# Kernel optimization log

Measured on AMD Instinct MI355X. Metric: run time of the kernel, lower is better.

Reference implementation:

```python
import jax, jax.numpy as jnp
import numpy as np

EP = 1e-4
MAX_ITER = 100
L = [512, 512]          # context lengths
C = 256                 # padded feature dim == total_dim
HEADS = 2


def nonsat_activation(x, ep=EP, max_iter=MAX_ITER):
    # Fixed-point iteration y <- (2y^3/3 + x)/(y^2+1), y0 = x.
    # Matches torch version: iterate on detached values, final update uses live x.
    xd = jax.lax.stop_gradient(x)
    f = lambda y: (2.0 * y ** 3 / 3.0 + xd) / (y ** 2 + 1.0)

    def cond(s):
        y, y_new, i = s
        return jnp.logical_and(jnp.mean(jnp.abs(y_new - y)) > ep, i <= max_iter)

    def body(s):
        y, y_new, i = s
        return (y_new, f(y_new), i + 1)

    y_prev, _, _ = jax.lax.while_loop(cond, body, (xd, f(xd), 0))
    y_prev = jax.lax.stop_gradient(y_prev)
    # final (returned) update, differentiable w.r.t. x only
    return (2.0 * y_prev ** 3 / 3.0 + x) / (y_prev ** 2 + 1.0)


def setup_inputs() -> dict:
    key = jax.random.key(0)
    k1, k2, k3 = jax.random.split(key, 3)
    x1 = jax.random.normal(k1, (32, 512, 256), dtype=jnp.float32)
    x2 = jax.random.normal(k2, (32, 512, 192), dtype=jnp.float32)
    # xavier_normal_ for U: std = sqrt(2/(fan_in+fan_out)) = sqrt(2/512) = 1/16
    U = jax.random.normal(k3, (HEADS, C, C), dtype=jnp.float32) * (1.0 / 16.0)
    return {"x1": x1, "x2": x2, "U": U}


def reference(x1, x2, U):
    # pad contexts to common feature dim C (zeros on the right)
    contexts = [x1, jnp.pad(x2, ((0, 0), (0, 0), (0, C - x2.shape[-1])))]
    q = sum(L)
    scaling = C ** (-0.5)
    M = jnp.concatenate(contexts, axis=1)  # (B, q, C)

    # mask uses sizes = L[1:] with blocks starting at offset 0 (faithful quirk)
    mask_mul = jnp.ones((q, q), dtype=jnp.float32).at[:L[1], :L[1]].set(0.0)

    h_reps = []
    mask_add = None
    for h in range(HEADS):
        # K[b,i,j] = sum_{c,d} M[b,i,c] U[h,c,d] M[b,j,d]
        K = jnp.einsum('bic,cd,bjd->bij', M, U[h], M) * scaling
        K = nonsat_activation(K)
        if mask_add is None:  # cached after head 0, reused for later heads
            mask_add = jnp.zeros((q, q), dtype=jnp.float32).at[:L[1], :L[1]].set(jnp.min(K))
        K_hat = K * mask_mul + mask_add
        cols = jnp.max(K_hat, axis=1)   # (B, q) max over rows per column
        rows = jnp.max(K_hat, axis=2)   # (B, q) max over cols per row
        alpha = rows + cols             # (B, q)
        reps = []
        offset = 0
        for i, Ci in enumerate(contexts):
            a = alpha[:, offset:offset + L[i]]          # (B, l_i)
            offset += L[i]
            wt = jax.nn.softmax(a, axis=1)              # (B, l_i)
            r = jnp.einsum('bl,blc->bc', wt, Ci)        # (B, C)
            reps.append(r)
        h_reps.append(jnp.stack(reps, axis=1))          # (B, N, C)
    return jnp.stack(h_reps, axis=0)                    # (heads, B, N, C)
```

## Files before the change

### kernel.cpp

```cpp
#include <hip/hip_runtime.h>
#include <math.h>

typedef _Float16 h16;
typedef h16  h16x8 __attribute__((ext_vector_type(8)));
typedef h16  h16x4 __attribute__((ext_vector_type(4)));
typedef float f32x4 __attribute__((ext_vector_type(4)));

#define MH_OFF   ((size_t)0)
#define ML_OFF   (MH_OFF + 16777216)
#define UHT_OFF  (ML_OFF + 16777216)
#define ULT_OFF  (UHT_OFF + 262144)
#define RMA_OFF  (ULT_OFF + 262144)
#define RMH_OFF  (RMA_OFF + 262144)
#define PCM_OFF  (RMH_OFF + 262144)
#define M0_OFF   (PCM_OFF + 4194304)

__device__ __forceinline__ float nonsat(float x) {
    float y = x;
#pragma unroll
    for (int i = 0; i < 24; ++i) {
        float y2 = y * y;
        y = fmaf(0.66666667f * y, y2, x) / (y2 + 1.0f);
    }
    return y;
}

__device__ __forceinline__ int fkey(float f) {
    const int i = __float_as_int(f);
    return (i >= 0) ? i : (i ^ 0x7fffffff);
}
__device__ __forceinline__ float funkey(int k) {
    return __int_as_float((k >= 0) ? k : (k ^ 0x7fffffff));
}

__global__ void k_prep(const float* __restrict__ x1, const float* __restrict__ x2,
                       const float* __restrict__ U, h16* __restrict__ MH,
                       h16* __restrict__ ML, h16* __restrict__ UHt,
                       h16* __restrict__ ULt, int* __restrict__ m0key,
                       float* __restrict__ out) {
    const int gid = blockIdx.x * 256 + threadIdx.x;
    if (blockIdx.x < 8192) {
        const int g  = gid;
        const int d4 = (g & 63) * 4;
        const int j  = (g >> 6) & 1023;
        const int b  = g >> 16;
        float v[4];
        if (j < 512) {
            const float4 p = *(const float4*)(x1 + ((size_t)(b * 512 + j) * 256 + d4));
            v[0] = p.x; v[1] = p.y; v[2] = p.z; v[3] = p.w;
        } else if (d4 < 192) {
            const float4 p = *(const float4*)(x2 +
                (size_t)(b * 512 + (j - 512)) * 192 + d4);
            v[0] = p.x; v[1] = p.y; v[2] = p.z; v[3] = p.w;
        } else {
            v[0] = v[1] = v[2] = v[3] = 0.0f;
        }
        h16x4 hh, ll;
#pragma unroll
        for (int k = 0; k < 4; ++k) {
            const h16 hi = (h16)v[k];
            hh[k] = hi;
            ll[k] = (h16)(v[k] - (float)hi);
        }
        const size_t o = (size_t)g * 4;
        *(h16x4*)&MH[o] = hh;
        *(h16x4*)&ML[o] = ll;
    } else if (blockIdx.x < 8320) {
        const int g  = gid - 8192 * 256;
        const int c4 = (g & 63) * 4;
        const int d  = (g >> 6) & 255;
        const int h  = g >> 14;
        h16x4 hh, ll;
#pragma unroll
        for (int k = 0; k < 4; ++k) {
            const float v = U[((size_t)h * 256 + c4 + k) * 256 + d] * 4.0f;
            const h16 hi = (h16)v;
            hh[k] = hi;
            ll[k] = (h16)(v - (float)hi);
        }
        const size_t o = ((size_t)h * 256 + d) * 256 + c4;
        *(h16x4*)&UHt[o] = hh;
        *(h16x4*)&ULt[o] = ll;
    } else {
        const int z = gid - 8320 * 256;
        out[z] = 0.0f;
        if (z == 0) *m0key = 0x7fffffff;
    }
}

__device__ __forceinline__ void stage_b(const h16* __restrict__ MH,
                                        const h16* __restrict__ ML,
                                        h16* sBf, int buf, int b, int jt,
                                        int jtile, int kc, int t, int w) {
    const int jrow0 = jt * 512 + jtile * 256;
    const int c = (t & 3) ^ ((t >> 3) & 3);
#pragma unroll
    for (int g = 0; g < 2; ++g) {
        const size_t src = (size_t)(b * 1024 + jrow0 + g * 128 + (t >> 2)) * 256
                           + kc * 32 + c * 8;
        h16* dH = sBf + (size_t)(buf * 2 + 0) * 8192 + g * 4096 + w * 512;
        h16* dL = sBf + (size_t)(buf * 2 + 1) * 8192 + g * 4096 + w * 512;
        __builtin_amdgcn_global_load_lds(
            (const __attribute__((address_space(1))) void*)(MH + src),
            (__attribute__((address_space(3))) void*)dH, 16, 0, 0);
        __builtin_amdgcn_global_load_lds(
            (const __attribute__((address_space(1))) void*)(ML + src),
            (__attribute__((address_space(3))) void*)dL, 16, 0, 0);
    }
}

__global__ __launch_bounds__(512, 2)
void k_main(const h16* __restrict__ MH, const h16* __restrict__ ML,
            const h16* __restrict__ UHt, const h16* __restrict__ ULt,
            float* __restrict__ rmax_all, float* __restrict__ rmax_hi,
            float* __restrict__ pcm, int* __restrict__ m0key) {
    __shared__ __align__(16) h16 sP[2][64 * 256];
    __shared__ __align__(16) h16 sB[2 * 2 * 8192];
    __shared__ float red[1024 + 8];
    __shared__ float scm[2][512];

    const int n    = blockIdx.x;
    const int x    = n & 7;
    const int s    = n >> 3;
    const int b    = x + 8 * (s >> 5);
    const int h    = (s >> 4) & 1;
    const int rblk = s & 15;
    const int hb   = h * 32 + b;
    const int r0   = rblk * 64;
    const int t    = threadIdx.x;
    const int w    = t >> 6;
    const int l    = t & 63;
    const int q    = l >> 4;
    const int ln   = l & 15;
    const int wr   = w >> 2;
    const int wj   = w & 3;

    const int jts    = (h == 1 && rblk < 8) ? 1 : 0;
    const int Usteps = (2 - jts) * 16;

    stage_b(MH, ML, sB, 0, b, jts, 0, 0, t, w);

    {
        const int wrA = w >> 2, wcA = w & 3;
        f32x4 accA[2][4];
        const f32x4 z4 = {0.f, 0.f, 0.f, 0.f};
#pragma unroll
        for (int i = 0; i < 2; ++i)
#pragma unroll
            for (int j2 = 0; j2 < 4; ++j2) accA[i][j2] = z4;

        for (int kc = 0; kc < 8; ++kc) {
            const int c0 = kc * 32;
            h16x8 aH[2], aL[2], bH[4], bL[4];
#pragma unroll
            for (int ti = 0; ti < 2; ++ti) {
                const size_t off =
                    (size_t)(b * 1024 + r0 + wrA * 32 + ti * 16 + ln) * 256 + c0 + q * 8;
                aH[ti] = *(const h16x8*)&MH[off];
                aL[ti] = *(const h16x8*)&ML[off];
            }
#pragma unroll
            for (int tj = 0; tj < 4; ++tj) {
                const size_t off =
                    (size_t)(h * 256 + wcA * 64 + tj * 16 + ln) * 256 + c0 + q * 8;
                bH[tj] = *(const h16x8*)&UHt[off];
                bL[tj] = *(const h16x8*)&ULt[off];
            }
#pragma unroll
            for (int ti = 0; ti < 2; ++ti)
#pragma unroll
                for (int tj = 0; tj < 4; ++tj)
                    accA[ti][tj] = __builtin_amdgcn_mfma_f32_16x16x32_f16(
                        aH[ti], bH[tj], accA[ti][tj], 0, 0, 0);
#pragma unroll
            for (int ti = 0; ti < 2; ++ti)
#pragma unroll
                for (int tj = 0; tj < 4; ++tj)
                    accA[ti][tj] = __builtin_amdgcn_mfma_f32_16x16x32_f16(
                        aL[ti], bH[tj], accA[ti][tj], 0, 0, 0);
#pragma unroll
            for (int ti = 0; ti < 2; ++ti)
#pragma unroll
                for (int tj = 0; tj < 4; ++tj)
                    accA[ti][tj] = __builtin_amdgcn_mfma_f32_16x16x32_f16(
                        aH[ti], bL[tj], accA[ti][tj], 0, 0, 0);
        }
#pragma unroll
        for (int ti = 0; ti < 2; ++ti)
#pragma unroll
            for (int tj = 0; tj < 4; ++tj)
#pragma unroll
                for (int reg = 0; reg < 4; ++reg) {
                    const int r = wrA * 32 + ti * 16 + q * 4 + reg;
                    const int d = wcA * 64 + tj * 16 + ln;
                    const float v = accA[ti][tj][reg];
                    const h16 hi = (h16)v;
                    const h16 lo = (h16)(v - (float)hi);
                    const int off = r * 256 + (((d >> 3) ^ (r & 7)) << 3) + (d & 7);
                    sP[0][off] = hi;
                    sP[1][off] = lo;
                }
    }
    __syncthreads();

    float gmin = INFINITY;
    float rm[2][4];
    f32x4 acc[2][4];
    const f32x4 z4 = {0.f, 0.f, 0.f, 0.f};
    int cur = 0;

#pragma unroll 1
    for (int u = 0; u < Usteps; ++u) {
        const int jt    = jts + (u >> 4);
        const int jtile = (u >> 3) & 1;
        const int kc    = u & 7;
        const bool dored = (rblk >= 8) || (jt == 1);

        if (u + 1 < Usteps) {
            const int u1 = u + 1;
            stage_b(MH, ML, sB, cur ^ 1, b, jts + (u1 >> 4), (u1 >> 3) & 1,
                    u1 & 7, t, w);
        }
        if (kc == 0) {
#pragma unroll
            for (int i = 0; i < 2; ++i)
#pragma unroll
                for (int j2 = 0; j2 < 4; ++j2) acc[i][j2] = z4;
            if (jtile == 0) {
#pragma unroll
                for (int i = 0; i < 2; ++i)
#pragma unroll
                    for (int j2 = 0; j2 < 4; ++j2) rm[i][j2] = -INFINITY;
            }
        }

        h16x8 aH[2], aL[2], bH[4], bL[4];
#pragma unroll
        for (int ti = 0; ti < 2; ++ti) {
            const int r = wr * 32 + ti * 16 + ln;
            const int g = ((kc * 4 + q) ^ (r & 7)) * 8;
            aH[ti] = *(const h16x8*)&sP[0][r * 256 + g];
            aL[ti] = *(const h16x8*)&sP[1][r * 256 + g];
        }
#pragma unroll
        for (int tj = 0; tj < 4; ++tj) {
            const int jr = wj * 64 + tj * 16 + ln;
            const int cp = (q ^ ((jr >> 1) & 3)) * 8;
            bH[tj] = *(const h16x8*)&sB[(size_t)(cur * 2 + 0) * 8192 + jr * 32 + cp];
            bL[tj] = *(const h16x8*)&sB[(size_t)(cur * 2 + 1) * 8192 + jr * 32 + cp];
        }
#pragma unroll
        for (int tj = 0; tj < 4; ++tj)
#pragma unroll
            for (int ti = 0; ti < 2; ++ti)
                acc[ti][tj] = __builtin_amdgcn_mfma_f32_16x16x32_f16(
                    aH[ti], bH[tj], acc[ti][tj], 0, 0, 0);
#pragma unroll
        for (int tj = 0; tj < 4; ++tj)
#pragma unroll
            for (int ti = 0; ti < 2; ++ti)
                acc[ti][tj] = __builtin_amdgcn_mfma_f32_16x16x32_f16(
                    aL[ti], bH[tj], acc[ti][tj], 0, 0, 0);
#pragma unroll
        for (int tj = 0; tj < 4; ++tj)
#pragma unroll
            for (int ti = 0; ti < 2; ++ti)
                acc[ti][tj] = __builtin_amdgcn_mfma_f32_16x16x32_f16(
                    aH[ti], bL[tj], acc[ti][tj], 0, 0, 0);

        if (kc == 7) {
            if (dored) {
#pragma unroll
                for (int ti = 0; ti < 2; ++ti)
#pragma unroll
                    for (int reg = 0; reg < 4; ++reg) {
                        float m = acc[ti][0][reg];
#pragma unroll
                        for (int tj = 1; tj < 4; ++tj) m = fmaxf(m, acc[ti][tj][reg]);
                        m = fmaxf(m, __shfl_xor(m, 1));
                        m = fmaxf(m, __shfl_xor(m, 2));
                        m = fmaxf(m, __shfl_xor(m, 4));
                        m = fmaxf(m, __shfl_xor(m, 8));
                        rm[ti][reg] = fmaxf(rm[ti][reg], m);
                    }
                if (jtile == 1) {
#pragma unroll
                    for (int ti = 0; ti < 2; ++ti)
#pragma unroll
                        for (int reg = 0; reg < 4; ++reg)
                            if (ln == 0)
                                red[(jt * 8 + w) * 64 + wr * 32 + ti * 16 +
                                    q * 4 + reg] = rm[ti][reg];
                }
#pragma unroll
                for (int tj = 0; tj < 4; ++tj) {
                    float m = -INFINITY;
#pragma unroll
                    for (int ti = 0; ti < 2; ++ti)
#pragma unroll
                        for (int reg = 0; reg < 4; ++reg)
                            m = fmaxf(m, acc[ti][tj][reg]);
                    m = fmaxf(m, __shfl_xor(m, 16));
                    m = fmaxf(m, __shfl_xor(m, 32));
                    if (q == 0)
                        scm[wr][jtile * 256 + wj * 64 + tj * 16 + ln] = m;
                }
            }
            if (h == 0) {
#pragma unroll
                for (int ti = 0; ti < 2; ++ti)
#pragma unroll
                    for (int tj = 0; tj < 4; ++tj)
#pragma unroll
                        for (int reg = 0; reg < 4; ++reg)
                            gmin = fminf(gmin, acc[ti][tj][reg]);
            }
        }
        __syncthreads();
        cur ^= 1;
        if ((u & 15) == 15 && dored) {
            const float v = fmaxf(scm[0][t], scm[1][t]);
            pcm[(size_t)(hb * 16 + rblk) * 1024 + jt * 512 + t] = v * 0.015625f;
        }
    }

#pragma unroll
    for (int off = 1; off < 64; off <<= 1) gmin = fminf(gmin, __shfl_xor(gmin, off));
    if (l == 0) red[1024 + w] = gmin;
    __syncthreads();

    if (t < 64) {
        const int wrr = t >> 5;
        float hh = -INFINITY;
#pragma unroll
        for (int w2 = 0; w2 < 4; ++w2)
            hh = fmaxf(hh, red[(8 + wrr * 4 + w2) * 64 + t]);
        if (rblk < 8) {
            rmax_hi[(size_t)hb * 1024 + r0 + t] = hh * 0.015625f;
        } else {
            float a = hh;
#pragma unroll
            for (int w2 = 0; w2 < 4; ++w2)
                a = fmaxf(a, red[(wrr * 4 + w2) * 64 + t]);
            rmax_all[(size_t)hb * 1024 + r0 + t] = a * 0.015625f;
        }
    }
    if (t == 0 && hb < 32) {
        float g4 = red[1024];
#pragma unroll
        for (int i = 1; i < 8; ++i) g4 = fminf(g4, red[1024 + i]);
        atomicMin(m0key, fkey(g4 * 0.015625f));
    }
}

__global__ __launch_bounds__(256)
void k_fin(const float* __restrict__ rmax_all, const float* __restrict__ rmax_hi,
           const float* __restrict__ pcm, const int* __restrict__ m0key,
           const float* __restrict__ x1, const float* __restrict__ x2,
           float* __restrict__ out) {
    __shared__ float wv[512];
    __shared__ float sm[4], ss[4];
    const int blk   = blockIdx.x;
    const int chunk = blk & 1;
    const int seg   = (blk >> 1) & 1;
    const int hb    = blk >> 2;
    const int b     = hb & 31;
    const int t     = threadIdx.x;
    const float m0  = funkey(*m0key);

    float a2[2];
#pragma unroll
    for (int half = 0; half < 2; ++half) {
        const int i = seg * 512 + half * 256 + t;
        float rraw;
        if (seg == 0) rraw = fmaxf(m0, rmax_hi[(size_t)hb * 1024 + i]);
        else          rraw = rmax_all[(size_t)hb * 1024 + i];
        float call = -INFINITY, chi = -INFINITY;
#pragma unroll
        for (int rb = 0; rb < 16; ++rb) {
            const float v = pcm[(size_t)(hb * 16 + rb) * 1024 + i];
            call = fmaxf(call, v);
            if (rb >= 8) chi = fmaxf(chi, v);
        }
        const float craw = (seg == 0) ? fmaxf(m0, chi) : call;
        a2[half] = nonsat(rraw) + nonsat(craw);
    }
    const float a0 = a2[0], a1 = a2[1];

    float m = fmaxf(a0, a1);
#pragma unroll
    for (int off = 1; off < 64; off <<= 1) m = fmaxf(m, __shfl_xor(m, off));
    if ((t & 63) == 0) sm[t >> 6] = m;
    __syncthreads();
    const float amax = fmaxf(fmaxf(sm[0], sm[1]), fmaxf(sm[2], sm[3]));

    const float e0 = __expf(a0 - amax), e1 = __expf(a1 - amax);
    wv[t] = e0; wv[t + 256] = e1;
    float s = e0 + e1;
#pragma unroll
    for (int off = 1; off < 64; off <<= 1) s += __shfl_xor(s, off);
    if ((t & 63) == 0) ss[t >> 6] = s;
    __syncthreads();
    const float inv = 1.0f / (ss[0] + ss[1] + ss[2] + ss[3]);

    const int lo = chunk * 256;
    float acc = 0.0f;
    if (seg == 0) {
        const float* xp = x1 + ((size_t)b * 512 + lo) * 256 + t;
#pragma unroll 4
        for (int l = 0; l < 256; ++l)
            acc = fmaf(wv[lo + l], xp[(size_t)l * 256], acc);
        atomicAdd(&out[(hb * 2 + seg) * 256 + t], acc * inv);
    } else if (t < 192) {
        const float* xp = x2 + ((size_t)b * 512 + lo) * 192 + t;
#pragma unroll 4
        for (int l = 0; l < 256; ++l)
            acc = fmaf(wv[lo + l], xp[(size_t)l * 192], acc);
        atomicAdd(&out[(hb * 2 + seg) * 256 + t], acc * inv);
    }
}

extern "C" void kernel_launch(void* const* d_in, const int* in_sizes, int n_in,
                              void* d_out, int out_size, void* d_ws, size_t ws_size,
                              hipStream_t stream) {
    const float* x1 = (const float*)d_in[0];
    const float* x2 = (const float*)d_in[1];
    const float* U  = (const float*)d_in[2];
    float* out = (float*)d_out;
    char* wsb  = (char*)d_ws;

    h16*   MHp  = (h16*)(wsb + MH_OFF);
    h16*   MLp  = (h16*)(wsb + ML_OFF);
    h16*   UHt  = (h16*)(wsb + UHT_OFF);
    h16*   ULt  = (h16*)(wsb + ULT_OFF);
    float* rma  = (float*)(wsb + RMA_OFF);
    float* rmh  = (float*)(wsb + RMH_OFF);
    float* pcm  = (float*)(wsb + PCM_OFF);
    int*   m0k  = (int*)(wsb + M0_OFF);

    hipLaunchKernelGGL(k_prep, dim3(8448), dim3(256), 0, stream, x1, x2, U,
                       MHp, MLp, UHt, ULt, m0k, out);
    hipLaunchKernelGGL(k_main, dim3(1024), dim3(512), 0, stream, MHp, MLp,
                       UHt, ULt, rma, rmh, pcm, m0k);
    hipLaunchKernelGGL(k_fin,  dim3(256),  dim3(256), 0, stream, rma, rmh,
                       pcm, m0k, x1, x2, out);
}
```

Measured before the change: 314.4 us.

## Deepen B-tile pipeline to four LDS stages with smaller j-tiles and vmcnt waits

```diff
diff --git a/kernel.cpp b/kernel.cpp
--- a/kernel.cpp
+++ b/kernel.cpp
@@ -90,23 +90,22 @@
 
 __device__ __forceinline__ void stage_b(const h16* __restrict__ MH,
                                         const h16* __restrict__ ML,
-                                        h16* sBf, int buf, int b, int jt,
-                                        int jtile, int kc, int t, int w) {
-    const int jrow0 = jt * 512 + jtile * 256;
+                                        h16* __restrict__ sBf, int b, int jts,
+                                        int u, int t) {
+    const int jt    = jts + (u >> 5);
+    const int jtile = (u >> 3) & 3;
+    const int kc    = u & 7;
+    const int jrow0 = jt * 512 + jtile * 128;
     const int c = (t & 3) ^ ((t >> 3) & 3);
-#pragma unroll
-    for (int g = 0; g < 2; ++g) {
-        const size_t src = (size_t)(b * 1024 + jrow0 + g * 128 + (t >> 2)) * 256
-                           + kc * 32 + c * 8;
-        h16* dH = sBf + (size_t)(buf * 2 + 0) * 8192 + g * 4096 + w * 512;
-        h16* dL = sBf + (size_t)(buf * 2 + 1) * 8192 + g * 4096 + w * 512;
-        __builtin_amdgcn_global_load_lds(
-            (const __attribute__((address_space(1))) void*)(MH + src),
-            (__attribute__((address_space(3))) void*)dH, 16, 0, 0);
-        __builtin_amdgcn_global_load_lds(
-            (const __attribute__((address_space(1))) void*)(ML + src),
-            (__attribute__((address_space(3))) void*)dL, 16, 0, 0);
-    }
+    const size_t src = (size_t)(b * 1024 + jrow0 + (t >> 2)) * 256 + kc * 32 + c * 8;
+    h16* dH = sBf + (size_t)(u & 3) * 8192 + t * 8;
+    h16* dL = sBf + (size_t)(u & 3) * 8192 + 4096 + t * 8;
+    __builtin_amdgcn_global_load_lds(
+        (const __attribute__((address_space(1))) void*)(MH + src),
+        (__attribute__((address_space(3))) void*)dH, 16, 0, 0);
+    __builtin_amdgcn_global_load_lds(
+        (const __attribute__((address_space(1))) void*)(ML + src),
+        (__attribute__((address_space(3))) void*)dL, 16, 0, 0);
 }
 
 __global__ __launch_bounds__(512, 2)
@@ -115,7 +114,7 @@
             float* __restrict__ rmax_all, float* __restrict__ rmax_hi,
             float* __restrict__ pcm, int* __restrict__ m0key) {
     __shared__ __align__(16) h16 sP[2][64 * 256];
-    __shared__ __align__(16) h16 sB[2 * 2 * 8192];
+    __shared__ __align__(16) h16 sB[4 * 8192];
     __shared__ float red[1024 + 8];
     __shared__ float scm[2][512];
 
@@ -136,9 +135,11 @@
     const int wj   = w & 3;
 
     const int jts    = (h == 1 && rblk < 8) ? 1 : 0;
-    const int Usteps = (2 - jts) * 16;
-
-    stage_b(MH, ML, sB, 0, b, jts, 0, 0, t, w);
+    const int Usteps = (2 - jts) * 32;
+
+    stage_b(MH, ML, sB, b, jts, 0, t);
+    stage_b(MH, ML, sB, b, jts, 1, t);
+    stage_b(MH, ML, sB, b, jts, 2, t);
 
     {
         const int wrA = w >> 2, wcA = w & 3;
@@ -205,28 +206,31 @@
 
     float gmin = INFINITY;
     float rm[2][4];
-    f32x4 acc[2][4];
+    f32x4 acc[2][2];
     const f32x4 z4 = {0.f, 0.f, 0.f, 0.f};
-    int cur = 0;
 
 #pragma unroll 1
     for (int u = 0; u < Usteps; ++u) {
-        const int jt    = jts + (u >> 4);
-        const int jtile = (u >> 3) & 1;
-        const int kc    = u & 7;
+        const int kc = u & 7;
+        const int jt = jts + (u >> 5);
         const bool dored = (rblk >= 8) || (jt == 1);
 
-        if (u + 1 < Usteps) {
-            const int u1 = u + 1;
-            stage_b(MH, ML, sB, cur ^ 1, b, jts + (u1 >> 4), (u1 >> 3) & 1,
-                    u1 & 7, t, w);
-        }
+        if (u) {
+            if (u + 3 <= Usteps)      asm volatile("s_waitcnt vmcnt(4)" ::: "memory");
+            else if (u + 2 <= Usteps) asm volatile("s_waitcnt vmcnt(2)" ::: "memory");
+            else                      asm volatile("s_waitcnt vmcnt(0)" ::: "memory");
+            asm volatile("s_waitcnt lgkmcnt(0)" ::: "memory");
+            __builtin_amdgcn_s_barrier();
+            __builtin_amdgcn_sched_barrier(0);
+        }
+        if (u + 3 < Usteps) stage_b(MH, ML, sB, b, jts, u + 3, t);
+
         if (kc == 0) {
 #pragma unroll
             for (int i = 0; i < 2; ++i)
 #pragma unroll
-                for (int j2 = 0; j2 < 4; ++j2) acc[i][j2] = z4;
-            if (jtile == 0) {
+                for (int j2 = 0; j2 < 2; ++j2) acc[i][j2] = z4;
+            if ((u & 31) == 0) {
 #pragma unroll
                 for (int i = 0; i < 2; ++i)
 #pragma unroll
@@ -234,7 +238,7 @@
             }
         }
 
-        h16x8 aH[2], aL[2], bH[4], bL[4];
+        h16x8 aH[2], aL[2], bH[2], bL[2];
 #pragma unroll
         for (int ti = 0; ti < 2; ++ti) {
             const int r = wr * 32 + ti * 16 + ln;
@@ -242,27 +246,28 @@
             aH[ti] = *(const h16x8*)&sP[0][r * 256 + g];
             aL[ti] = *(const h16x8*)&sP[1][r * 256 + g];
         }
-#pragma unroll
-        for (int tj = 0; tj < 4; ++tj) {
-            const int jr = wj * 64 + tj * 16 + ln;
+        const h16* sBb = &sB[(size_t)(u & 3) * 8192];
+#pragma unroll
+        for (int tj = 0; tj < 2; ++tj) {
+            const int jr = wj * 32 + tj * 16 + ln;
             const int cp = (q ^ ((jr >> 1) & 3)) * 8;
-            bH[tj] = *(const h16x8*)&sB[(size_t)(cur * 2 + 0) * 8192 + jr * 32 + cp];
-            bL[tj] = *(const h16x8*)&sB[(size_t)(cur * 2 + 1) * 8192 + jr * 32 + cp];
-        }
-#pragma unroll
-        for (int tj = 0; tj < 4; ++tj)
+            bH[tj] = *(const h16x8*)&sBb[jr * 32 + cp];
+            bL[tj] = *(const h16x8*)&sBb[4096 + jr * 32 + cp];
+        }
+#pragma unroll
+        for (int tj = 0; tj < 2; ++tj)
 #pragma unroll
             for (int ti = 0; ti < 2; ++ti)
                 acc[ti][tj] = __builtin_amdgcn_mfma_f32_16x16x32_f16(
                     aH[ti], bH[tj], acc[ti][tj], 0, 0, 0);
 #pragma unroll
-        for (int tj = 0; tj < 4; ++tj)
+        for (int tj = 0; tj < 2; ++tj)
 #pragma unroll
             for (int ti = 0; ti < 2; ++ti)
                 acc[ti][tj] = __builtin_amdgcn_mfma_f32_16x16x32_f16(
                     aL[ti], bH[tj], acc[ti][tj], 0, 0, 0);
 #pragma unroll
-        for (int tj = 0; tj < 4; ++tj)
+        for (int tj = 0; tj < 2; ++tj)
 #pragma unroll
             for (int ti = 0; ti < 2; ++ti)
                 acc[ti][tj] = __builtin_amdgcn_mfma_f32_16x16x32_f16(
@@ -270,20 +275,19 @@
 
         if (kc == 7) {
             if (dored) {
+                const int jtile = (u >> 3) & 3;
 #pragma unroll
                 for (int ti = 0; ti < 2; ++ti)
 #pragma unroll
                     for (int reg = 0; reg < 4; ++reg) {
-                        float m = acc[ti][0][reg];
-#pragma unroll
-                        for (int tj = 1; tj < 4; ++tj) m = fmaxf(m, acc[ti][tj][reg]);
+                        float m = fmaxf(acc[ti][0][reg], acc[ti][1][reg]);
                         m = fmaxf(m, __shfl_xor(m, 1));
                         m = fmaxf(m, __shfl_xor(m, 2));
                         m = fmaxf(m, __shfl_xor(m, 4));
                         m = fmaxf(m, __shfl_xor(m, 8));
                         rm[ti][reg] = fmaxf(rm[ti][reg], m);
                     }
-                if (jtile == 1) {
+                if ((u & 31) == 31) {
 #pragma unroll
                     for (int ti = 0; ti < 2; ++ti)
 #pragma unroll
@@ -293,7 +297,7 @@
                                     q * 4 + reg] = rm[ti][reg];
                 }
 #pragma unroll
-                for (int tj = 0; tj < 4; ++tj) {
+                for (int tj = 0; tj < 2; ++tj) {
                     float m = -INFINITY;
 #pragma unroll
                     for (int ti = 0; ti < 2; ++ti)
@@ -303,24 +307,25 @@
                     m = fmaxf(m, __shfl_xor(m, 16));
                     m = fmaxf(m, __shfl_xor(m, 32));
                     if (q == 0)
-                        scm[wr][jtile * 256 + wj * 64 + tj * 16 + ln] = m;
+                        scm[wr][jtile * 128 + wj * 32 + tj * 16 + ln] = m;
                 }
             }
             if (h == 0) {
 #pragma unroll
                 for (int ti = 0; ti < 2; ++ti)
 #pragma unroll
-                    for (int tj = 0; tj < 4; ++tj)
+                    for (int tj = 0; tj < 2; ++tj)
 #pragma unroll
                         for (int reg = 0; reg < 4; ++reg)
                             gmin = fminf(gmin, acc[ti][tj][reg]);
             }
         }
-        __syncthreads();
-        cur ^= 1;
-        if ((u & 15) == 15 && dored) {
-            const float v = fmaxf(scm[0][t], scm[1][t]);
-            pcm[(size_t)(hb * 16 + rblk) * 1024 + jt * 512 + t] = v * 0.015625f;
+        if ((u & 31) == 31) {
+            asm volatile("s_waitcnt lgkmcnt(0)" ::: "memory");
+            __builtin_amdgcn_s_barrier();
+            if (dored)
+                pcm[(size_t)(hb * 16 + rblk) * 1024 + jt * 512 + t] =
+                    fmaxf(scm[0][t], scm[1][t]) * 0.015625f;
         }
     }
 
@@ -330,18 +335,17 @@
     __syncthreads();
 
     if (t < 64) {
-        const int wrr = t >> 5;
         float hh = -INFINITY;
 #pragma unroll
-        for (int w2 = 0; w2 < 4; ++w2)
-            hh = fmaxf(hh, red[(8 + wrr * 4 + w2) * 64 + t]);
+        for (int w2 = 0; w2 < 8; ++w2)
+            hh = fmaxf(hh, red[(8 + w2) * 64 + t]);
         if (rblk < 8) {
             rmax_hi[(size_t)hb * 1024 + r0 + t] = hh * 0.015625f;
         } else {
             float a = hh;
 #pragma unroll
-            for (int w2 = 0; w2 < 4; ++w2)
-                a = fmaxf(a, red[(wrr * 4 + w2) * 64 + t]);
+            for (int w2 = 0; w2 < 8; ++w2)
+                a = fmaxf(a, red[w2 * 64 + t]);
             rmax_all[(size_t)hb * 1024 + r0 + t] = a * 0.015625f;
         }
     }
```

Result: slower. 367.0 us (+16.7%).
